# Kernel optimization log

Hardware: AMD Instinct MI355X
Metric: run time of the kernel (lower is better)

The kernel has to match this reference:

```python
import jax, jax.numpy as jnp
import numpy as np

B, N, C, T, K = 32, 4096, 768, 1000, 20

def setup_inputs() -> dict:
    key = jax.random.key(0)
    k1, k2, k3, k4 = jax.random.split(key, 4)
    g_feat = jax.random.normal(k1, (B, 1, C), dtype=jnp.float32)
    inp = jax.random.normal(k2, (B, N, C), dtype=jnp.float32)
    tau = jax.random.uniform(k3, (1,), dtype=jnp.float32)
    text_embeddings = jax.random.normal(k4, (T, C), dtype=jnp.float32) * 0.01
    return {"g_feat": g_feat, "input": inp, "tau": tau, "text_embeddings": text_embeddings}


def reference(g_feat, input, tau, text_embeddings):
    feat = input  # [B, N, C]
    # 1x1 conv of global feature against text embeddings -> class logits [B, T]
    vg_logit = jnp.einsum('bc,tc->bt', g_feat[:, 0, :], text_embeddings)
    # top-20 candidate categories per image
    _, indices = jax.lax.top_k(vg_logit, K)              # [B, K]
    agg_text_features = text_embeddings[indices]          # [B, K, C] gather
    # per-pixel logits against the 20 gathered text embeddings
    seg_logit = jnp.exp(tau[0]) * jnp.einsum('bkc,bnc->bkn', agg_text_features, feat)  # [B, K, N]
    # hard (straight-through) softmax over candidate axis (dim=-2)
    y_soft = jax.nn.softmax(seg_logit, axis=-2)
    idx = jnp.argmax(seg_logit, axis=-2)                  # [B, N]
    y_hard = jnp.moveaxis(jax.nn.one_hot(idx, K, dtype=seg_logit.dtype), -1, -2)  # [B, K, N]
    attn = y_hard - jax.lax.stop_gradient(y_soft) + y_soft
    # normalize over pixel axis (assign_eps = 1.0)
    assign_attn = attn / (jnp.sum(attn, axis=-1, keepdims=True) + 1.0)
    # combine: [B, N, K] @ [B, K, C] -> [B, N, C]
    text_grids = jnp.einsum('bkn,bkc->bnc', assign_attn, agg_text_features)
    return text_grids
```

## Files before the change

### kernel.cpp

```cpp
#include <hip/hip_runtime.h>
#include <cfloat>

#define B_ 32
#define N_ 4096
#define C_ 768
#define T_ 1000
#define K_ 20

#define PXB 256
#define PHC 32
#define NPH (C_/PHC)
#define ECH 160
#define EPADC 184
#define GAP_TH 1e-3f
#define MAXF 16384

typedef float f32x4 __attribute__((ext_vector_type(4)));

__global__ __launch_bounds__(256) void k1_logits(const float* __restrict__ g_feat,
                                                 const float* __restrict__ text,
                                                 double* __restrict__ logits,
                                                 int* __restrict__ cnt,
                                                 int* __restrict__ flagcnt) {
    int b = blockIdx.x;
    int wid = threadIdx.x >> 6, lane = threadIdx.x & 63;
    int t = blockIdx.y * 4 + wid;
    if (b == 0 && blockIdx.y == 0) {
        for (int i = threadIdx.x; i < B_ * K_; i += 256) cnt[i] = 0;
        if (threadIdx.x == 0) flagcnt[0] = 0;
    }
    const float* g = g_feat + b * C_;
    const float* e = text + t * C_;
    double s = 0.0;
    #pragma unroll
    for (int j = 0; j < 12; ++j) {
        int c = lane + 64 * j;
        s += (double)g[c] * (double)e[c];
    }
    #pragma unroll
    for (int m = 32; m; m >>= 1) s += __shfl_xor(s, m);
    if (lane == 0) logits[b * T_ + t] = s;
}

__global__ __launch_bounds__(256) void k1b_topk(const double* __restrict__ logits,
                                                const float* __restrict__ text,
                                                float* __restrict__ agg,
                                                int* __restrict__ sel) {
    __shared__ double ll[T_];
    __shared__ double rv[256];
    __shared__ int    ri[256];
    __shared__ int    ssel[K_];
    int b = blockIdx.x, tid = threadIdx.x;
    for (int t = tid; t < T_; t += 256) ll[t] = logits[b * T_ + t];
    __syncthreads();
    for (int j = 0; j < K_; ++j) {
        double bv = -DBL_MAX; int bi = 0;
        for (int t = tid; t < T_; t += 256) {
            double v = ll[t];
            if (v > bv) { bv = v; bi = t; }
        }
        rv[tid] = bv; ri[tid] = bi;
        __syncthreads();
        for (int s = 128; s; s >>= 1) {
            if (tid < s) {
                double ov = rv[tid + s]; int oi = ri[tid + s];
                if (ov > rv[tid] || (ov == rv[tid] && oi < ri[tid])) { rv[tid] = ov; ri[tid] = oi; }
            }
            __syncthreads();
        }
        if (tid == 0) { ssel[j] = ri[0]; ll[ri[0]] = -DBL_MAX; }
        __syncthreads();
    }
    if (tid < K_) sel[b * K_ + tid] = ssel[tid];
    for (int i = tid; i < K_ * C_; i += 256) {
        int j = i / C_, c = i - j * C_;
        agg[b * K_ * C_ + i] = text[ssel[j] * C_ + c];
    }
}

__global__ __launch_bounds__(256) void k2_argmax(const float* __restrict__ feat,
                                                 const float* __restrict__ agg,
                                                 int* __restrict__ kidx,
                                                 int* __restrict__ cnt,
                                                 int* __restrict__ flagcnt,
                                                 int* __restrict__ flaglist) {
    __shared__ float fbuf[2][PXB * PHC];
    __shared__ float ebuf[2][EPADC * 4];
    __shared__ int scnt[K_];
    int bx = blockIdx.x;
    int b = bx >> 4, tile = bx & 15;
    int n0 = tile * PXB;
    int tid = threadIdx.x, wid = tid >> 6, lane = tid & 63;
    if (tid < K_) scnt[tid] = 0;
    __syncthreads();

    const float* fb = feat + ((size_t)b * N_ + n0) * C_;
    const float* eb = agg + b * (K_ * C_);

    int rsub = lane >> 3;
    int slot = lane & 7;
    int ec = wid * 40 + lane;
    int ecc = ec < ECH ? ec : (ECH - 1);
    const float* esrc_base = eb + (ecc >> 3) * C_ + 4 * (ecc & 7);

    auto stage = [&](int p, int s) {
        int c0 = p * PHC;
        #pragma unroll
        for (int i = 0; i < 8; ++i) {
            int row = wid * 64 + i * 8 + rsub;
            const float* g = fb + ((size_t)row * C_ + c0 + 4 * (slot ^ rsub));
            float* d = &fbuf[s][(wid * 64 + i * 8) * PHC];
            __builtin_amdgcn_global_load_lds((const __attribute__((address_space(1))) void*)g,
                                             (__attribute__((address_space(3))) void*)d, 16, 0, 0);
        }
        {
            const float* g = esrc_base + c0;
            float* d = &ebuf[s][wid * 40 * 4];
            __builtin_amdgcn_global_load_lds((const __attribute__((address_space(1))) void*)g,
                                             (__attribute__((address_space(3))) void*)d, 16, 0, 0);
        }
    };

    float acc[K_];
    #pragma unroll
    for (int k = 0; k < K_; ++k) acc[k] = 0.f;

    stage(0, 0);

    int r7 = tid & 7;
    #pragma unroll 1
    for (int p = 0; p < NPH; ++p) {
        int s = p & 1;
        if (p + 1 < NPH) {
            stage(p + 1, s ^ 1);
            asm volatile("s_waitcnt vmcnt(9)" ::: "memory");
        } else {
            asm volatile("s_waitcnt vmcnt(0)" ::: "memory");
        }
        asm volatile("s_barrier" ::: "memory");

        const float* rowp = &fbuf[s][tid * PHC];
        f32x4 f[8];
        #pragma unroll
        for (int j = 0; j < 8; ++j)
            f[j] = *(const f32x4*)(rowp + 4 * (j ^ r7));
        const float* ep = &ebuf[s][0];
        #pragma unroll
        for (int k = 0; k < K_; ++k) {
            float a = acc[k];
            #pragma unroll
            for (int j = 0; j < 8; ++j) {
                f32x4 e = *(const f32x4*)(ep + k * PHC + 4 * j);
                a = fmaf(f[j].x, e.x, a);
                a = fmaf(f[j].y, e.y, a);
                a = fmaf(f[j].z, e.z, a);
                a = fmaf(f[j].w, e.w, a);
            }
            acc[k] = a;
        }
        asm volatile("s_barrier" ::: "memory");
    }

    float m1 = acc[0]; int i1 = 0; float m2 = -FLT_MAX;
    #pragma unroll
    for (int k = 1; k < K_; ++k) {
        float v = acc[k];
        if (v > m1) { m2 = m1; m1 = v; i1 = k; }
        else if (v > m2) m2 = v;
    }
    int n = n0 + tid;
    kidx[b * N_ + n] = i1;
    atomicAdd(&scnt[i1], 1);
    if (m1 - m2 < GAP_TH) {
        int pos = atomicAdd(flagcnt, 1);
        if (pos < MAXF) flaglist[pos] = b * N_ + n;
    }
    __syncthreads();
    if (tid < K_) atomicAdd(&cnt[b * K_ + tid], scnt[tid]);
}

__global__ __launch_bounds__(256) void k25_refine(const float* __restrict__ feat,
                                                  const float* __restrict__ agg,
                                                  int* __restrict__ kidx,
                                                  int* __restrict__ cnt,
                                                  const int* __restrict__ flagcnt,
                                                  const int* __restrict__ flaglist) {
    int wid = threadIdx.x >> 6, lane = threadIdx.x & 63;
    int wg = blockIdx.x * 4 + wid;
    int nf = flagcnt[0]; if (nf > MAXF) nf = MAXF;
    for (int e = wg; e < nf; e += gridDim.x * 4) {
        int pix = flaglist[e];
        int b = pix >> 12;
        const float* fr = feat + (size_t)pix * C_;
        const float* ebase = agg + b * K_ * C_;
        double fd[12];
        #pragma unroll
        for (int j = 0; j < 12; ++j) fd[j] = (double)fr[lane + 64 * j];
        double best = -DBL_MAX; int bi = 0;
        for (int k = 0; k < K_; ++k) {
            const float* er = ebase + k * C_;
            double s = 0.0;
            #pragma unroll
            for (int j = 0; j < 12; ++j) s += fd[j] * (double)er[lane + 64 * j];
            #pragma unroll
            for (int m = 32; m; m >>= 1) s += __shfl_xor(s, m);
            if (s > best) { best = s; bi = k; }
        }
        if (lane == 0) {
            int old = kidx[pix];
            if (old != bi) {
                kidx[pix] = bi;
                atomicSub(&cnt[b * K_ + old], 1);
                atomicAdd(&cnt[b * K_ + bi], 1);
            }
        }
    }
}

__global__ __launch_bounds__(256) void k4_out(const float* __restrict__ agg,
                                              const int* __restrict__ cnt,
                                              const int* __restrict__ kidx,
                                              float* __restrict__ out) {
    int wid = threadIdx.x >> 6, lane = threadIdx.x & 63;
    int wg = blockIdx.x * 4 + wid;
    int base = wg * 16;
    int b = base >> 12;
    int kk[16];
    #pragma unroll
    for (int i = 0; i < 16; ++i) kk[i] = kidx[base + i];
    float sc[16];
    #pragma unroll
    for (int i = 0; i < 16; ++i) sc[i] = 1.0f / ((float)cnt[b * K_ + kk[i]] + 1.0f);
    const f32x4* agg4 = (const f32x4*)agg;
    f32x4* out4 = (f32x4*)out;
    #pragma unroll
    for (int i = 0; i < 16; ++i) {
        const f32x4* a4 = agg4 + (size_t)(b * K_ + kk[i]) * (C_ / 4);
        f32x4* o4 = out4 + (size_t)(base + i) * (C_ / 4);
        #pragma unroll
        for (int j = 0; j < 3; ++j) {
            f32x4 v = a4[lane + 64 * j];
            v *= sc[i];
            __builtin_nontemporal_store(v, &o4[lane + 64 * j]);
        }
    }
}

extern "C" void kernel_launch(void* const* d_in, const int* in_sizes, int n_in,
                              void* d_out, int out_size, void* d_ws, size_t ws_size,
                              hipStream_t stream) {
    const float* g_feat = (const float*)d_in[0];
    const float* feat   = (const float*)d_in[1];
    const float* text   = (const float*)d_in[3];
    float* out = (float*)d_out;

    char* ws = (char*)d_ws;
    double* logits = (double*)(ws + 0);
    float*  agg    = (float*) (ws + 262144);
    int*    sel    = (int*)   (ws + 2228224);
    int*    cnt    = (int*)   (ws + 2230784);
    int*    flagc  = (int*)   (ws + 2233344);
    int*    flagl  = (int*)   (ws + 2233408);
    int*    kidx   = (int*)   (ws + 2301504);

    k1_logits<<<dim3(32, 250), 256, 0, stream>>>(g_feat, text, logits, cnt, flagc);
    k1b_topk<<<32, 256, 0, stream>>>(logits, text, agg, sel);
    k2_argmax<<<32 * 16, 256, 0, stream>>>(feat, agg, kidx, cnt, flagc, flagl);
    k25_refine<<<64, 256, 0, stream>>>(feat, agg, kidx, cnt, flagc, flagl);
    k4_out<<<2048, 256, 0, stream>>>(agg, cnt, kidx, out);
}
```

Before: 304.4 us.

## Triple-buffer argmax with two pixels per thread, warp-level top-k, finer output grid

The argmax kernel now runs 128 threads per block, and each thread accumulates two pixels so every text-embedding LDS read is reused twice. Channel phases shrink to 16, the staging ring grows from two to three buffers with a new XOR swizzle, and each buffer is prefetched two phases ahead to hide more load latency. Top-k selection moves to a single wavefront using register-held logits and shuffle reductions, which removes the shared-memory tree and its many barriers. The output kernel handles 8 pixels per wave on twice as many blocks, trading per-wave work for more parallelism at the cost of fewer threads per block in the main kernel.

```diff
diff --git a/kernel.cpp b/kernel.cpp
--- a/kernel.cpp
+++ b/kernel.cpp
@@ -8,10 +8,8 @@
 #define K_ 20
 
 #define PXB 256
-#define PHC 32
+#define PHC 16
 #define NPH (C_/PHC)
-#define ECH 160
-#define EPADC 184
 #define GAP_TH 1e-3f
 #define MAXF 16384
 
@@ -46,31 +44,36 @@
                                                 const float* __restrict__ text,
                                                 float* __restrict__ agg,
                                                 int* __restrict__ sel) {
-    __shared__ double ll[T_];
-    __shared__ double rv[256];
-    __shared__ int    ri[256];
-    __shared__ int    ssel[K_];
-    int b = blockIdx.x, tid = threadIdx.x;
-    for (int t = tid; t < T_; t += 256) ll[t] = logits[b * T_ + t];
+    __shared__ int ssel[K_];
+    int b = blockIdx.x, tid = threadIdx.x, lane = tid & 63;
+    if (tid < 64) {
+        double v[16];
+        #pragma unroll
+        for (int j = 0; j < 16; ++j) {
+            int t = lane + 64 * j;
+            v[j] = (t < T_) ? logits[b * T_ + t] : -DBL_MAX;
+        }
+        for (int it = 0; it < K_; ++it) {
+            double bv = -DBL_MAX; int bi = 0x7fffffff;
+            #pragma unroll
+            for (int j = 0; j < 16; ++j) {
+                int t = lane + 64 * j;
+                if (v[j] > bv) { bv = v[j]; bi = t; }
+            }
+            #pragma unroll
+            for (int m = 32; m; m >>= 1) {
+                double ov = __shfl_xor(bv, m); int oi = __shfl_xor(bi, m);
+                if (ov > bv || (ov == bv && oi < bi)) { bv = ov; bi = oi; }
+            }
+            if (lane == 0) ssel[it] = bi;
+            #pragma unroll
+            for (int j = 0; j < 16; ++j) {
+                int t = lane + 64 * j;
+                if (t == bi) v[j] = -DBL_MAX;
+            }
+        }
+    }
     __syncthreads();
-    for (int j = 0; j < K_; ++j) {
-        double bv = -DBL_MAX; int bi = 0;
-        for (int t = tid; t < T_; t += 256) {
-            double v = ll[t];
-            if (v > bv) { bv = v; bi = t; }
-        }
-        rv[tid] = bv; ri[tid] = bi;
-        __syncthreads();
-        for (int s = 128; s; s >>= 1) {
-            if (tid < s) {
-                double ov = rv[tid + s]; int oi = ri[tid + s];
-                if (ov > rv[tid] || (ov == rv[tid] && oi < ri[tid])) { rv[tid] = ov; ri[tid] = oi; }
-            }
-            __syncthreads();
-        }
-        if (tid == 0) { ssel[j] = ri[0]; ll[ri[0]] = -DBL_MAX; }
-        __syncthreads();
-    }
     if (tid < K_) sel[b * K_ + tid] = ssel[tid];
     for (int i = tid; i < K_ * C_; i += 256) {
         int j = i / C_, c = i - j * C_;
@@ -78,14 +81,14 @@
     }
 }
 
-__global__ __launch_bounds__(256) void k2_argmax(const float* __restrict__ feat,
+__global__ __launch_bounds__(128) void k2_argmax(const float* __restrict__ feat,
                                                  const float* __restrict__ agg,
                                                  int* __restrict__ kidx,
                                                  int* __restrict__ cnt,
                                                  int* __restrict__ flagcnt,
                                                  int* __restrict__ flaglist) {
-    __shared__ float fbuf[2][PXB * PHC];
-    __shared__ float ebuf[2][EPADC * 4];
+    __shared__ float fbuf[3][PXB * PHC];
+    __shared__ float ebuf[3][512];
     __shared__ int scnt[K_];
     int bx = blockIdx.x;
     int b = bx >> 4, tile = bx & 15;
@@ -97,83 +100,93 @@
     const float* fb = feat + ((size_t)b * N_ + n0) * C_;
     const float* eb = agg + b * (K_ * C_);
 
-    int rsub = lane >> 3;
-    int slot = lane & 7;
-    int ec = wid * 40 + lane;
-    int ecc = ec < ECH ? ec : (ECH - 1);
-    const float* esrc_base = eb + (ecc >> 3) * C_ + 4 * (ecc & 7);
-
-    auto stage = [&](int p, int s) {
-        int c0 = p * PHC;
-        #pragma unroll
-        for (int i = 0; i < 8; ++i) {
-            int row = wid * 64 + i * 8 + rsub;
-            const float* g = fb + ((size_t)row * C_ + c0 + 4 * (slot ^ rsub));
-            float* d = &fbuf[s][(wid * 64 + i * 8) * PHC];
+    int se = wid * 64 + lane;
+    int ce = se < 80 ? se : 79;
+    const float* esrc = eb + (ce >> 2) * C_ + (ce & 3) * 4;
+
+    auto stage = [&](int p, int bufi) {
+        #pragma unroll
+        for (int ii = 0; ii < 8; ++ii) {
+            int s = (wid * 8 + ii) * 64 + lane;
+            int c = s ^ ((s >> 3) & 7);
+            int px = c >> 2, j = c & 3;
+            const float* g = fb + (size_t)px * C_ + p * PHC + j * 4;
+            float* d = &fbuf[bufi][(wid * 8 + ii) * 256];
             __builtin_amdgcn_global_load_lds((const __attribute__((address_space(1))) void*)g,
                                              (__attribute__((address_space(3))) void*)d, 16, 0, 0);
         }
         {
-            const float* g = esrc_base + c0;
-            float* d = &ebuf[s][wid * 40 * 4];
+            const float* g = esrc + p * PHC;
+            float* d = &ebuf[bufi][wid * 256];
             __builtin_amdgcn_global_load_lds((const __attribute__((address_space(1))) void*)g,
                                              (__attribute__((address_space(3))) void*)d, 16, 0, 0);
         }
     };
 
-    float acc[K_];
-    #pragma unroll
-    for (int k = 0; k < K_; ++k) acc[k] = 0.f;
+    float acc0[K_], acc1[K_];
+    #pragma unroll
+    for (int k = 0; k < K_; ++k) { acc0[k] = 0.f; acc1[k] = 0.f; }
 
     stage(0, 0);
-
-    int r7 = tid & 7;
+    stage(1, 1);
+
+    int p0 = tid, p1 = tid + 128;
     #pragma unroll 1
     for (int p = 0; p < NPH; ++p) {
-        int s = p & 1;
-        if (p + 1 < NPH) {
-            stage(p + 1, s ^ 1);
+        int bufi = p % 3;
+        if (p + 2 < NPH) {
+            stage(p + 2, (p + 2) % 3);
+            asm volatile("s_waitcnt vmcnt(18)" ::: "memory");
+        } else if (p + 1 < NPH) {
             asm volatile("s_waitcnt vmcnt(9)" ::: "memory");
         } else {
             asm volatile("s_waitcnt vmcnt(0)" ::: "memory");
         }
         asm volatile("s_barrier" ::: "memory");
 
-        const float* rowp = &fbuf[s][tid * PHC];
-        f32x4 f[8];
-        #pragma unroll
-        for (int j = 0; j < 8; ++j)
-            f[j] = *(const f32x4*)(rowp + 4 * (j ^ r7));
-        const float* ep = &ebuf[s][0];
+        const float* fB = fbuf[bufi];
+        const float* eB = ebuf[bufi];
+        f32x4 F0[4], F1[4];
+        #pragma unroll
+        for (int j = 0; j < 4; ++j) {
+            int c0 = p0 * 4 + j, h0 = c0 ^ ((c0 >> 3) & 7);
+            F0[j] = *(const f32x4*)(fB + h0 * 4);
+            int c1 = p1 * 4 + j, h1 = c1 ^ ((c1 >> 3) & 7);
+            F1[j] = *(const f32x4*)(fB + h1 * 4);
+        }
         #pragma unroll
         for (int k = 0; k < K_; ++k) {
-            float a = acc[k];
-            #pragma unroll
-            for (int j = 0; j < 8; ++j) {
-                f32x4 e = *(const f32x4*)(ep + k * PHC + 4 * j);
-                a = fmaf(f[j].x, e.x, a);
-                a = fmaf(f[j].y, e.y, a);
-                a = fmaf(f[j].z, e.z, a);
-                a = fmaf(f[j].w, e.w, a);
-            }
-            acc[k] = a;
+            float a0 = acc0[k], a1 = acc1[k];
+            #pragma unroll
+            for (int j = 0; j < 4; ++j) {
+                f32x4 e = *(const f32x4*)(eB + (k * 4 + j) * 4);
+                a0 = fmaf(F0[j].x, e.x, a0); a0 = fmaf(F0[j].y, e.y, a0);
+                a0 = fmaf(F0[j].z, e.z, a0); a0 = fmaf(F0[j].w, e.w, a0);
+                a1 = fmaf(F1[j].x, e.x, a1); a1 = fmaf(F1[j].y, e.y, a1);
+                a1 = fmaf(F1[j].z, e.z, a1); a1 = fmaf(F1[j].w, e.w, a1);
+            }
+            acc0[k] = a0; acc1[k] = a1;
         }
         asm volatile("s_barrier" ::: "memory");
     }
 
-    float m1 = acc[0]; int i1 = 0; float m2 = -FLT_MAX;
-    #pragma unroll
-    for (int k = 1; k < K_; ++k) {
-        float v = acc[k];
-        if (v > m1) { m2 = m1; m1 = v; i1 = k; }
-        else if (v > m2) m2 = v;
-    }
-    int n = n0 + tid;
-    kidx[b * N_ + n] = i1;
-    atomicAdd(&scnt[i1], 1);
-    if (m1 - m2 < GAP_TH) {
-        int pos = atomicAdd(flagcnt, 1);
-        if (pos < MAXF) flaglist[pos] = b * N_ + n;
+    #pragma unroll
+    for (int q = 0; q < 2; ++q) {
+        float* acc = q ? acc1 : acc0;
+        float m1 = acc[0]; int i1 = 0; float m2 = -FLT_MAX;
+        #pragma unroll
+        for (int k = 1; k < K_; ++k) {
+            float v = acc[k];
+            if (v > m1) { m2 = m1; m1 = v; i1 = k; }
+            else if (v > m2) m2 = v;
+        }
+        int n = n0 + tid + q * 128;
+        kidx[b * N_ + n] = i1;
+        atomicAdd(&scnt[i1], 1);
+        if (m1 - m2 < GAP_TH) {
+            int pos = atomicAdd(flagcnt, 1);
+            if (pos < MAXF) flaglist[pos] = b * N_ + n;
+        }
     }
     __syncthreads();
     if (tid < K_) atomicAdd(&cnt[b * K_ + tid], scnt[tid]);
@@ -223,18 +236,18 @@
                                               float* __restrict__ out) {
     int wid = threadIdx.x >> 6, lane = threadIdx.x & 63;
     int wg = blockIdx.x * 4 + wid;
-    int base = wg * 16;
+    int base = wg * 8;
     int b = base >> 12;
-    int kk[16];
-    #pragma unroll
-    for (int i = 0; i < 16; ++i) kk[i] = kidx[base + i];
-    float sc[16];
-    #pragma unroll
-    for (int i = 0; i < 16; ++i) sc[i] = 1.0f / ((float)cnt[b * K_ + kk[i]] + 1.0f);
+    int kk[8];
+    #pragma unroll
+    for (int i = 0; i < 8; ++i) kk[i] = kidx[base + i];
+    float sc[8];
+    #pragma unroll
+    for (int i = 0; i < 8; ++i) sc[i] = 1.0f / ((float)cnt[b * K_ + kk[i]] + 1.0f);
     const f32x4* agg4 = (const f32x4*)agg;
     f32x4* out4 = (f32x4*)out;
     #pragma unroll
-    for (int i = 0; i < 16; ++i) {
+    for (int i = 0; i < 8; ++i) {
         const f32x4* a4 = agg4 + (size_t)(b * K_ + kk[i]) * (C_ / 4);
         f32x4* o4 = out4 + (size_t)(base + i) * (C_ / 4);
         #pragma unroll
@@ -265,7 +278,7 @@
 
     k1_logits<<<dim3(32, 250), 256, 0, stream>>>(g_feat, text, logits, cnt, flagc);
     k1b_topk<<<32, 256, 0, stream>>>(logits, text, agg, sel);
-    k2_argmax<<<32 * 16, 256, 0, stream>>>(feat, agg, kidx, cnt, flagc, flagl);
+    k2_argmax<<<32 * 16, 128, 0, stream>>>(feat, agg, kidx, cnt, flagc, flagl);
     k25_refine<<<64, 256, 0, stream>>>(feat, agg, kidx, cnt, flagc, flagl);
-    k4_out<<<2048, 256, 0, stream>>>(agg, cnt, kidx, out);
-}
+    k4_out<<<4096, 256, 0, stream>>>(agg, cnt, kidx, out);
+}
```

New measurement: 299.6 us. No clear change (-1.6%).
